# Performance work log

Measured on AMD Instinct MI355X. Metric: run time of the kernel, lower is better.

## Reference

```python
import jax, jax.numpy as jnp
import numpy as np

N = 100000          # total nodes
E = 600000          # edges (before self-loops)
DIN = 768           # input_dim
H = 128             # hidden_dim
G = 100             # nodes per graph (node 0 of each graph is the query node)


def _xavier(key, fan_in, fan_out):
    lim = float(np.sqrt(6.0 / (fan_in + fan_out)))
    return jax.random.uniform(key, (fan_in, fan_out), jnp.float32, -lim, lim)


def setup_inputs() -> dict:
    key = jax.random.key(0)
    ks = jax.random.split(key, 8)
    x = jax.random.normal(ks[0], (N, DIN), jnp.float32)
    edge_src = jax.random.randint(ks[1], (E,), 0, N, jnp.int32)
    edge_dst = jax.random.randint(ks[2], (E,), 0, N, jnp.int32)
    ids = np.arange(N)
    batch_vec = jnp.asarray(ids // G, jnp.int32)          # graph id per node
    tool_idx = jnp.asarray(np.nonzero(ids % G != 0)[0], jnp.int32)   # node_type==1
    query_idx = jnp.asarray(np.nonzero(ids % G == 0)[0], jnp.int32)  # node_type==0
    W_align = _xavier(ks[3], DIN, H); b_align = jnp.zeros((H,), jnp.float32)
    W1 = _xavier(ks[4], H, H); b1 = jnp.zeros((H,), jnp.float32)
    W2 = _xavier(ks[5], H, H); b2 = jnp.zeros((H,), jnp.float32)
    W_out = _xavier(ks[6], H, 1); b_out = jnp.zeros((1,), jnp.float32)
    return dict(x=x, edge_src=edge_src, edge_dst=edge_dst, batch_vec=batch_vec,
                tool_idx=tool_idx, query_idx=query_idx,
                W_align=W_align, b_align=b_align, W1=W1, b1=b1, W2=W2, b2=b2,
                W_out=W_out, b_out=b_out)


def reference(x, edge_src, edge_dst, batch_vec, tool_idx, query_idx,
              W_align, b_align, W1, b1, W2, b2, W_out, b_out):
    n = x.shape[0]
    # GCNConv gcn_norm: add self-loops (weight 1), symmetric normalization.
    loop = jnp.arange(n, dtype=edge_src.dtype)
    src = jnp.concatenate([edge_src, loop])
    dst = jnp.concatenate([edge_dst, loop])
    w = jnp.ones(src.shape[0], x.dtype)
    deg = jax.ops.segment_sum(w, dst, num_segments=n)
    dinv = jnp.where(deg > 0, jax.lax.rsqrt(deg), 0.0)
    norm = dinv[src] * w * dinv[dst]                      # [E+N]

    h = x @ W_align + b_align                              # [N, H]
    for W, b in ((W1, b1), (W2, b2)):
        residual = h
        m = h @ W                                          # GCNConv linear (no bias)
        agg = jax.ops.segment_sum(m[src] * norm[:, None], dst, num_segments=n)
        h = jax.nn.relu(agg + b)                           # conv bias, then relu
        # dropout is identity at inference
        h = h + residual                                   # residual (shapes match)

    tool_logits = (h[tool_idx] @ W_out + b_out)[:, 0]
    query_logits = (h[query_idx] @ W_out + b_out)[:, 0]
    tool_batch_index = batch_vec[tool_idx]
    return tool_logits, query_logits, tool_batch_index
```

## Files before the change

kernel.cpp:

```cpp
#include <hip/hip_runtime.h>
#include <hip/hip_fp16.h>


#define HDIM 128

typedef short s16x8 __attribute__((ext_vector_type(8)));
typedef unsigned short u16;
typedef unsigned short u16x8 __attribute__((ext_vector_type(8)));
typedef float f32x4 __attribute__((ext_vector_type(4)));

__device__ inline void split2(float f, u16& hi, u16& lo) {
  unsigned u = __builtin_bit_cast(unsigned, f);
  hi = (u16)(u >> 16);
  float fh = __builtin_bit_cast(float, u & 0xFFFF0000u);
  float fl = f - fh;
  lo = (u16)(__builtin_bit_cast(unsigned, fl) >> 16);
}

__device__ inline u16 bf16rne(float f) {
  unsigned u = __builtin_bit_cast(unsigned, f);
  u += 0x7FFFu + ((u >> 16) & 1u);
  return (u16)(u >> 16);
}

__device__ inline s16x8 cvt8(f32x4 a, f32x4 b) {
  s16x8 r;
  r[0] = (short)bf16rne(a[0]); r[1] = (short)bf16rne(a[1]);
  r[2] = (short)bf16rne(a[2]); r[3] = (short)bf16rne(a[3]);
  r[4] = (short)bf16rne(b[0]); r[5] = (short)bf16rne(b[1]);
  r[6] = (short)bf16rne(b[2]); r[7] = (short)bf16rne(b[3]);
  return r;
}


__global__ __launch_bounds__(256) void k_prep(int* __restrict__ degi, int N,
                                              const int* __restrict__ tool_idx,
                                              const int* __restrict__ query_idx,
                                              const int* __restrict__ batch_vec,
                                              int* __restrict__ pos,
                                              float* __restrict__ out,
                                              int n_tool, int n_query,
                                              const float* __restrict__ Wa,
                                              const float* __restrict__ W1,
                                              const float* __restrict__ W2,
                                              u16* __restrict__ tha, u16* __restrict__ tla,
                                              u16* __restrict__ th1, u16* __restrict__ tl1,
                                              u16* __restrict__ th2, u16* __restrict__ tl2,
                                              int na, int n1) {
  int g = blockIdx.x * 256 + threadIdx.x;
  if (g < N) degi[g] = 0;
  int g1 = g - N;
  if (g1 >= 0 && g1 < n_tool) {
    int nd = tool_idx[g1];
    pos[nd] = g1;
    out[n_tool + n_query + g1] = (float)batch_vec[nd];
  } else if (g1 >= n_tool && g1 < n_tool + n_query) {
    int q = g1 - n_tool;
    pos[query_idx[q]] = n_tool + q;
  }
  int g2 = g - N - n_tool - n_query;
  if (g2 >= 0 && g2 < na + 2 * n1) {
    const float* W;
    u16 *th, *tl;
    int idx;
    if (g2 < na) { W = Wa; th = tha; tl = tla; idx = g2; }
    else if (g2 < na + n1) { W = W1; th = th1; tl = tl1; idx = g2 - na; }
    else { W = W2; th = th2; tl = tl2; idx = g2 - na - n1; }
    int n = idx & 127, k = idx >> 7;
    u16 h, l;
    split2(W[idx], h, l);
    int o = ((k >> 5) << 12) | (n << 5) | (k & 31);
    th[o] = h;
    tl[o] = l;
  }
}


__global__ __launch_bounds__(256) void k_count(const int* __restrict__ dst,
                                               int* __restrict__ degi, int E) {
  int g = blockIdx.x * 256 + threadIdx.x;
  if (g < E) atomicAdd(&degi[dst[g]], 1);
}

__global__ __launch_bounds__(256) void k_scan1(const int* __restrict__ in,
                                               int* __restrict__ out,
                                               int* __restrict__ bsum,
                                               float* __restrict__ dinv, int n) {
  __shared__ int s[256];
  int t = threadIdx.x, g = blockIdx.x * 256 + t;
  int v = (g < n) ? in[g] : 0;
  if (g < n) dinv[g] = rsqrtf((float)(v + 1));
  s[t] = v;
  for (int off = 1; off < 256; off <<= 1) {
    __syncthreads();
    int x = (t >= off) ? s[t - off] : 0;
    __syncthreads();
    s[t] += x;
  }
  if (g < n) out[g] = s[t] - v;
  if (t == 255) bsum[blockIdx.x] = s[255];
}

__global__ __launch_bounds__(512) void k_scan23(int* __restrict__ row_start,
                                                const int* __restrict__ bsum,
                                                int nb, int n, int total) {
  __shared__ int s[512];
  int t = threadIdx.x;
  int v = (t < nb) ? bsum[t] : 0;
  s[t] = v;
  for (int off = 1; off < 512; off <<= 1) {
    __syncthreads();
    int x = (t >= off) ? s[t - off] : 0;
    __syncthreads();
    s[t] += x;
  }
  __syncthreads();
  int g = blockIdx.x * 512 + t;
  int bi = g >> 8;
  int off = (bi == 0) ? 0 : s[bi - 1];
  if (g < n) row_start[g] += off;
  if (g == 0) row_start[n] = total;
}

__global__ __launch_bounds__(256) void k_fill(const int* __restrict__ src,
                                              const int* __restrict__ dst,
                                              const int* __restrict__ row_start,
                                              int* __restrict__ degi,
                                              const float* __restrict__ dinv,
                                              int* __restrict__ csr_src,
                                              float* __restrict__ csr_norm, int E) {
  int g = blockIdx.x * 256 + threadIdx.x;
  if (g < E) {
    int s = src[g], d = dst[g];
    int p = atomicSub(&degi[d], 1) - 1;
    int o = row_start[d] + p;
    csr_src[o] = s;
    csr_norm[o] = dinv[s] * dinv[d];
  }
}


template <int K, bool BIAS, bool OUTH>
__global__ __launch_bounds__(256) void k_gemm_bf(const float* __restrict__ A,
                                                 const u16* __restrict__ Bth,
                                                 const u16* __restrict__ Btl,
                                                 const float* __restrict__ bias,
                                                 void* __restrict__ Cv, int M) {
  __shared__ float Af[128][36];
  __shared__ u16 Bh[128][40];
  __shared__ u16 Bl[128][40];

  const int t = threadIdx.x;
  const int m0 = blockIdx.x << 7;
  const int lane = t & 63, w = t >> 6;
  const int wm = (w >> 1) << 6, wn = (w & 1) << 6;
  const int fr = lane & 15;
  const int fk = (lane >> 4) << 3;
  const int srow = t >> 1;
  const int scol = (t & 1) << 4;

  f32x4 acc[4][4] = {};
  const bool valid = (m0 + srow) < M;
  const float* arow = A + (size_t)(m0 + srow) * K + scol;

  f32x4 v0 = {}, v1 = {}, v2 = {}, v3 = {};
  if (valid) {
    v0 = *(const f32x4*)(arow + 0);
    v1 = *(const f32x4*)(arow + 4);
    v2 = *(const f32x4*)(arow + 8);
    v3 = *(const f32x4*)(arow + 12);
  }

  for (int kb = 0; kb < K; kb += 32) {
    *(f32x4*)&Af[srow][scol + 0] = v0;
    *(f32x4*)&Af[srow][scol + 4] = v1;
    *(f32x4*)&Af[srow][scol + 8] = v2;
    *(f32x4*)&Af[srow][scol + 12] = v3;

    {
      const u16* bsrc = Bth + ((size_t)(kb >> 5) << 12) + (t << 4);
      u16x8 p0 = *(const u16x8*)bsrc;
      u16x8 p1 = *(const u16x8*)(bsrc + 8);
      const u16* bsrc2 = Btl + ((size_t)(kb >> 5) << 12) + (t << 4);
      u16x8 q0 = *(const u16x8*)bsrc2;
      u16x8 q1 = *(const u16x8*)(bsrc2 + 8);
      int bn = t >> 1, bseg = (t & 1) << 4;
      *(u16x8*)&Bh[bn][bseg] = p0;
      *(u16x8*)&Bh[bn][bseg + 8] = p1;
      *(u16x8*)&Bl[bn][bseg] = q0;
      *(u16x8*)&Bl[bn][bseg + 8] = q1;
    }
    __syncthreads();

    if (valid && kb + 32 < K) {
      const float* ap = arow + kb + 32;
      v0 = *(const f32x4*)(ap + 0);
      v1 = *(const f32x4*)(ap + 4);
      v2 = *(const f32x4*)(ap + 8);
      v3 = *(const f32x4*)(ap + 12);
    }

    s16x8 ah[4], bh[4], bl[4];
#pragma unroll
    for (int i = 0; i < 4; ++i) {
      const float* ar = &Af[wm + (i << 4) + fr][fk];
      f32x4 a0 = *(const f32x4*)(ar + 0);
      f32x4 a1 = *(const f32x4*)(ar + 4);
      ah[i] = cvt8(a0, a1);
      bh[i] = *(const s16x8*)&Bh[wn + (i << 4) + fr][fk];
      bl[i] = *(const s16x8*)&Bl[wn + (i << 4) + fr][fk];
    }
#pragma unroll
    for (int i = 0; i < 4; ++i)
#pragma unroll
      for (int j = 0; j < 4; ++j) {
        acc[i][j] = __builtin_amdgcn_mfma_f32_16x16x32_bf16(ah[i], bh[j], acc[i][j], 0, 0, 0);
        acc[i][j] = __builtin_amdgcn_mfma_f32_16x16x32_bf16(ah[i], bl[j], acc[i][j], 0, 0, 0);
      }
    __syncthreads();
  }

  const int cr = (lane >> 4) << 2;
#pragma unroll
  for (int i = 0; i < 4; ++i) {
    int mbase = m0 + wm + (i << 4) + cr;
#pragma unroll
    for (int j = 0; j < 4; ++j) {
      int n = wn + (j << 4) + fr;
      float bv = BIAS ? bias[n] : 0.0f;
#pragma unroll
      for (int r = 0; r < 4; ++r) {
        if (mbase + r < M) {
          if (OUTH) {
            ((__half*)Cv)[(size_t)(mbase + r) * HDIM + n] =
                __float2half_rn(acc[i][j][r] + bv);
          } else {
            ((float*)Cv)[(size_t)(mbase + r) * HDIM + n] = acc[i][j][r] + bv;
          }
        }
      }
    }
  }
}


template <bool FINAL>
__global__ __launch_bounds__(256) void k_gather(const __half2* __restrict__ m2,
                                                float* __restrict__ h,
                                                const int* __restrict__ row_start,
                                                const int* __restrict__ csr_src,
                                                const float* __restrict__ csr_norm,
                                                const float* __restrict__ dinv,
                                                const float* __restrict__ bias,
                                                const float* __restrict__ Wout,
                                                const float* __restrict__ bout,
                                                const int* __restrict__ pos,
                                                float* __restrict__ out, int N) {
  int wid = (blockIdx.x * 256 + threadIdx.x) >> 6;
  int lane = threadIdx.x & 63;
  if (wid >= N) return;
  float di = dinv[wid];
  float sl = di * di;
  float2 mv = __half22float2(m2[(size_t)wid * 64 + lane]);
  float ax = mv.x * sl, ay = mv.y * sl;
  int e0 = row_start[wid], e1 = row_start[wid + 1];
  for (int base = e0; base < e1; base += 64) {
    int cnt = e1 - base;
    if (cnt > 64) cnt = 64;
    int sL = 0;
    float nL = 0.f;
    if (base + lane < e1) {
      sL = csr_src[base + lane];
      nL = csr_norm[base + lane];
    }
    for (int j = 0; j < cnt; ++j) {
      int s = __shfl(sL, j);
      float nr = __shfl(nL, j);
      float2 v = __half22float2(m2[(size_t)s * 64 + lane]);
      ax = fmaf(v.x, nr, ax);
      ay = fmaf(v.y, nr, ay);
    }
  }
  float2 bb = ((const float2*)bias)[lane];
  float2 hv = ((const float2*)h)[(size_t)wid * 64 + lane];
  float rx = fmaxf(ax + bb.x, 0.f) + hv.x;
  float ry = fmaxf(ay + bb.y, 0.f) + hv.y;
  if (FINAL) {
    float2 wv = ((const float2*)Wout)[lane];
    float s = rx * wv.x + ry * wv.y;
#pragma unroll
    for (int off = 32; off > 0; off >>= 1) s += __shfl_down(s, off);
    if (lane == 0) out[pos[wid]] = s + bout[0];
  } else {
    float2* h2 = (float2*)h;
    float2 r;
    r.x = rx;
    r.y = ry;
    h2[(size_t)wid * 64 + lane] = r;
  }
}


extern "C" void kernel_launch(void* const* d_in, const int* in_sizes, int n_in,
                              void* d_out, int out_size, void* d_ws, size_t ws_size,
                              hipStream_t stream) {
  const float* x        = (const float*)d_in[0];
  const int*   edge_src = (const int*)d_in[1];
  const int*   edge_dst = (const int*)d_in[2];
  const int*   batch_vec= (const int*)d_in[3];
  const int*   tool_idx = (const int*)d_in[4];
  const int*   query_idx= (const int*)d_in[5];
  const float* W_align  = (const float*)d_in[6];
  const float* b_align  = (const float*)d_in[7];
  const float* W1       = (const float*)d_in[8];
  const float* b1       = (const float*)d_in[9];
  const float* W2       = (const float*)d_in[10];
  const float* b2       = (const float*)d_in[11];
  const float* W_out    = (const float*)d_in[12];
  const float* b_out    = (const float*)d_in[13];

  const int N   = in_sizes[3];
  const int E   = in_sizes[1];
  const int DIN = in_sizes[0] / N;
  const int n_tool  = in_sizes[4];
  const int n_query = in_sizes[5];
  (void)n_in; (void)out_size; (void)ws_size;

  char* p = (char*)d_ws;
  auto alloc = [&](size_t bytes) {
    void* r = (void*)p;
    p += (bytes + 255) & ~(size_t)255;
    return r;
  };
  int*   degi      = (int*)alloc((size_t)N * 4);
  float* dinv      = (float*)alloc((size_t)N * 4);
  int*   row_start = (int*)alloc((size_t)(N + 1) * 4);
  int*   pos       = (int*)alloc((size_t)N * 4);
  int*   csr_src   = (int*)alloc((size_t)E * 4);
  float* csr_norm  = (float*)alloc((size_t)E * 4);
  float* h         = (float*)alloc((size_t)N * HDIM * 4);
  __half* m        = (__half*)alloc((size_t)N * HDIM * 2);
  int*   bsum      = (int*)alloc((size_t)1024 * 4);
  u16*   WthA      = (u16*)alloc((size_t)DIN * HDIM * 2);
  u16*   WtlA      = (u16*)alloc((size_t)DIN * HDIM * 2);
  u16*   Wth1      = (u16*)alloc((size_t)HDIM * HDIM * 2);
  u16*   Wtl1      = (u16*)alloc((size_t)HDIM * HDIM * 2);
  u16*   Wth2      = (u16*)alloc((size_t)HDIM * HDIM * 2);
  u16*   Wtl2      = (u16*)alloc((size_t)HDIM * HDIM * 2);

  const int nblkE = (E + 255) / 256;
  const int nblkN = (N + 255) / 256;
  const int na = DIN * HDIM, n1 = HDIM * HDIM;

  const int prepWork = N + n_tool + n_query + na + 2 * n1;
  k_prep<<<(prepWork + 255) / 256, 256, 0, stream>>>(
      degi, N, tool_idx, query_idx, batch_vec, pos, (float*)d_out, n_tool, n_query,
      W_align, W1, W2, WthA, WtlA, Wth1, Wtl1, Wth2, Wtl2, na, n1);

  k_count<<<nblkE, 256, 0, stream>>>(edge_dst, degi, E);
  k_scan1<<<nblkN, 256, 0, stream>>>(degi, row_start, bsum, dinv, N);
  k_scan23<<<(N + 511) / 512, 512, 0, stream>>>(row_start, bsum, nblkN, N, E);
  k_fill<<<nblkE, 256, 0, stream>>>(edge_src, edge_dst, row_start, degi, dinv,
                                    csr_src, csr_norm, E);

  const int gemmBlocks = (N + 127) / 128;
  const int waveBlocks = (N * 64 + 255) / 256;

  k_gemm_bf<768, true, false><<<gemmBlocks, 256, 0, stream>>>(
      x, WthA, WtlA, b_align, h, N);

  k_gemm_bf<128, false, true><<<gemmBlocks, 256, 0, stream>>>(
      h, Wth1, Wtl1, nullptr, m, N);
  k_gather<false><<<waveBlocks, 256, 0, stream>>>(
      (const __half2*)m, h, row_start, csr_src, csr_norm, dinv, b1,
      nullptr, nullptr, nullptr, nullptr, N);
  k_gemm_bf<128, false, true><<<gemmBlocks, 256, 0, stream>>>(
      h, Wth2, Wtl2, nullptr, m, N);
  k_gather<true><<<waveBlocks, 256, 0, stream>>>(
      (const __half2*)m, h, row_start, csr_src, csr_norm, dinv, b2,
      W_out, b_out, pos, (float*)d_out, N);
}
```

Baseline: 343.9 us.

## Drop LDS staging in GEMM; load MFMA fragments directly from pre-swizzled weights

New measurement: 404.3 us. 1.18x slower.

```diff
diff --git a/kernel.cpp b/kernel.cpp
--- a/kernel.cpp
+++ b/kernel.cpp
@@ -6,7 +6,6 @@
 
 typedef short s16x8 __attribute__((ext_vector_type(8)));
 typedef unsigned short u16;
-typedef unsigned short u16x8 __attribute__((ext_vector_type(8)));
 typedef float f32x4 __attribute__((ext_vector_type(4)));
 
 __device__ inline void split2(float f, u16& hi, u16& lo) {
@@ -69,7 +68,8 @@
     int n = idx & 127, k = idx >> 7;
     u16 h, l;
     split2(W[idx], h, l);
-    int o = ((k >> 5) << 12) | (n << 5) | (k & 31);
+    int o = ((k >> 5) << 12) | ((n >> 4) << 9) | (((k >> 3) & 3) << 7) |
+            ((n & 15) << 3) | (k & 7);
     th[o] = h;
     tl[o] = l;
   }
@@ -146,87 +146,50 @@
                                                  const u16* __restrict__ Btl,
                                                  const float* __restrict__ bias,
                                                  void* __restrict__ Cv, int M) {
-  __shared__ float Af[128][36];
-  __shared__ u16 Bh[128][40];
-  __shared__ u16 Bl[128][40];
-
   const int t = threadIdx.x;
-  const int m0 = blockIdx.x << 7;
   const int lane = t & 63, w = t >> 6;
-  const int wm = (w >> 1) << 6, wn = (w & 1) << 6;
   const int fr = lane & 15;
   const int fk = (lane >> 4) << 3;
-  const int srow = t >> 1;
-  const int scol = (t & 1) << 4;
-
-  f32x4 acc[4][4] = {};
-  const bool valid = (m0 + srow) < M;
-  const float* arow = A + (size_t)(m0 + srow) * K + scol;
-
-  f32x4 v0 = {}, v1 = {}, v2 = {}, v3 = {};
-  if (valid) {
-    v0 = *(const f32x4*)(arow + 0);
-    v1 = *(const f32x4*)(arow + 4);
-    v2 = *(const f32x4*)(arow + 8);
-    v3 = *(const f32x4*)(arow + 12);
-  }
+  const int m0 = blockIdx.x << 7;
+  const int r0 = m0 + (w << 5) + fr;
+  const int r1 = r0 + 16;
+  const bool ok0 = r0 < M, ok1 = r1 < M;
+  const float* a0p = A + (size_t)r0 * K + fk;
+  const float* a1p = A + (size_t)r1 * K + fk;
+
+  f32x4 acc[2][8] = {};
+
+  f32x4 x0 = {}, x1 = {}, y0 = {}, y1 = {};
+  if (ok0) { x0 = *(const f32x4*)(a0p); x1 = *(const f32x4*)(a0p + 4); }
+  if (ok1) { y0 = *(const f32x4*)(a1p); y1 = *(const f32x4*)(a1p + 4); }
 
   for (int kb = 0; kb < K; kb += 32) {
-    *(f32x4*)&Af[srow][scol + 0] = v0;
-    *(f32x4*)&Af[srow][scol + 4] = v1;
-    *(f32x4*)&Af[srow][scol + 8] = v2;
-    *(f32x4*)&Af[srow][scol + 12] = v3;
-
-    {
-      const u16* bsrc = Bth + ((size_t)(kb >> 5) << 12) + (t << 4);
-      u16x8 p0 = *(const u16x8*)bsrc;
-      u16x8 p1 = *(const u16x8*)(bsrc + 8);
-      const u16* bsrc2 = Btl + ((size_t)(kb >> 5) << 12) + (t << 4);
-      u16x8 q0 = *(const u16x8*)bsrc2;
-      u16x8 q1 = *(const u16x8*)(bsrc2 + 8);
-      int bn = t >> 1, bseg = (t & 1) << 4;
-      *(u16x8*)&Bh[bn][bseg] = p0;
-      *(u16x8*)&Bh[bn][bseg + 8] = p1;
-      *(u16x8*)&Bl[bn][bseg] = q0;
-      *(u16x8*)&Bl[bn][bseg + 8] = q1;
-    }
-    __syncthreads();
-
-    if (valid && kb + 32 < K) {
-      const float* ap = arow + kb + 32;
-      v0 = *(const f32x4*)(ap + 0);
-      v1 = *(const f32x4*)(ap + 4);
-      v2 = *(const f32x4*)(ap + 8);
-      v3 = *(const f32x4*)(ap + 12);
-    }
-
-    s16x8 ah[4], bh[4], bl[4];
-#pragma unroll
-    for (int i = 0; i < 4; ++i) {
-      const float* ar = &Af[wm + (i << 4) + fr][fk];
-      f32x4 a0 = *(const f32x4*)(ar + 0);
-      f32x4 a1 = *(const f32x4*)(ar + 4);
-      ah[i] = cvt8(a0, a1);
-      bh[i] = *(const s16x8*)&Bh[wn + (i << 4) + fr][fk];
-      bl[i] = *(const s16x8*)&Bl[wn + (i << 4) + fr][fk];
-    }
-#pragma unroll
-    for (int i = 0; i < 4; ++i)
-#pragma unroll
-      for (int j = 0; j < 4; ++j) {
-        acc[i][j] = __builtin_amdgcn_mfma_f32_16x16x32_bf16(ah[i], bh[j], acc[i][j], 0, 0, 0);
-        acc[i][j] = __builtin_amdgcn_mfma_f32_16x16x32_bf16(ah[i], bl[j], acc[i][j], 0, 0, 0);
-      }
-    __syncthreads();
+    s16x8 ah0 = cvt8(x0, x1);
+    s16x8 ah1 = cvt8(y0, y1);
+    if (kb + 32 < K) {
+      if (ok0) { x0 = *(const f32x4*)(a0p + kb + 32); x1 = *(const f32x4*)(a0p + kb + 36); }
+      if (ok1) { y0 = *(const f32x4*)(a1p + kb + 32); y1 = *(const f32x4*)(a1p + kb + 36); }
+    }
+    const u16* bhb = Bth + ((size_t)(kb >> 5) << 12) + (lane << 3);
+    const u16* blb = Btl + ((size_t)(kb >> 5) << 12) + (lane << 3);
+#pragma unroll
+    for (int j = 0; j < 8; ++j) {
+      s16x8 bh = *(const s16x8*)(bhb + ((size_t)j << 9));
+      s16x8 bl = *(const s16x8*)(blb + ((size_t)j << 9));
+      acc[0][j] = __builtin_amdgcn_mfma_f32_16x16x32_bf16(ah0, bh, acc[0][j], 0, 0, 0);
+      acc[0][j] = __builtin_amdgcn_mfma_f32_16x16x32_bf16(ah0, bl, acc[0][j], 0, 0, 0);
+      acc[1][j] = __builtin_amdgcn_mfma_f32_16x16x32_bf16(ah1, bh, acc[1][j], 0, 0, 0);
+      acc[1][j] = __builtin_amdgcn_mfma_f32_16x16x32_bf16(ah1, bl, acc[1][j], 0, 0, 0);
+    }
   }
 
   const int cr = (lane >> 4) << 2;
 #pragma unroll
-  for (int i = 0; i < 4; ++i) {
-    int mbase = m0 + wm + (i << 4) + cr;
-#pragma unroll
-    for (int j = 0; j < 4; ++j) {
-      int n = wn + (j << 4) + fr;
+  for (int i = 0; i < 2; ++i) {
+    int mbase = m0 + (w << 5) + (i << 4) + cr;
+#pragma unroll
+    for (int j = 0; j < 8; ++j) {
+      int n = (j << 4) + fr;
       float bv = BIAS ? bias[n] : 0.0f;
 #pragma unroll
       for (int r = 0; r < 4; ++r) {
```
